# Kernel tuning notes

Hardware: AMD Instinct MI355X
Metric: run time of the kernel (lower is better)

The kernel has to match this reference:

```python
import jax, jax.numpy as jnp
import numpy as np

DIM = 2048
N_HEADS = 32
N_KV_HEADS = 8
HEAD_DIM = DIM // N_HEADS  # 64
N_REP = N_HEADS // N_KV_HEADS  # 4
B, S = 1, 2048


def _rope(t, cos, sin):
    # t: (b, s, h, head_dim); cos/sin: (s, head_dim//2)
    tr = t.reshape(*t.shape[:-1], -1, 2)
    a, b = tr[..., 0], tr[..., 1]
    c = cos[None, :, None, :]
    s_ = sin[None, :, None, :]
    ra = a * c - b * s_
    rb = a * s_ + b * c
    return jnp.stack([ra, rb], axis=-1).reshape(t.shape)


def setup_inputs() -> dict:
    key = jax.random.key(0)
    ks = jax.random.split(key, 6)
    sc = 1.0 / np.sqrt(DIM)
    x = jax.random.normal(ks[0], (B, S, DIM), dtype=jnp.float32)
    wq = jax.random.normal(ks[1], (DIM, N_HEADS * HEAD_DIM), dtype=jnp.float32) * sc
    wk = jax.random.normal(ks[2], (DIM, N_KV_HEADS * HEAD_DIM), dtype=jnp.float32) * sc
    wv = jax.random.normal(ks[3], (DIM, N_KV_HEADS * HEAD_DIM), dtype=jnp.float32) * sc
    wo = jax.random.normal(ks[4], (N_HEADS * HEAD_DIM, DIM), dtype=jnp.float32) * sc
    # rotary frequencies (theta = 500000 as in Llama3)
    inv = 1.0 / (500000.0 ** (np.arange(0, HEAD_DIM, 2, dtype=np.float32) / HEAD_DIM))
    ang = np.arange(S, dtype=np.float32)[:, None] * inv[None, :]
    freqs_cos = jnp.asarray(np.cos(ang), dtype=jnp.float32)
    freqs_sin = jnp.asarray(np.sin(ang), dtype=jnp.float32)
    # causal additive mask
    mask = jnp.triu(jnp.full((S, S), -1e9, dtype=jnp.float32), k=1)
    return {"x": x, "wq": wq, "wk": wk, "wv": wv, "wo": wo,
            "freqs_cos": freqs_cos, "freqs_sin": freqs_sin, "mask": mask,
            "start_pos": 0}


def reference(x, wq, wk, wv, wo, freqs_cos, freqs_sin, mask, start_pos):
    b, s, _ = x.shape
    xq = (x @ wq).reshape(b, s, N_HEADS, HEAD_DIM)
    xk = (x @ wk).reshape(b, s, N_KV_HEADS, HEAD_DIM)
    xv = (x @ wv).reshape(b, s, N_KV_HEADS, HEAD_DIM)
    xq = _rope(xq, freqs_cos, freqs_sin)
    xk = _rope(xk, freqs_cos, freqs_sin)
    # GQA without repeat_interleave: view queries as (b, s, kv, rep, d)
    q = xq.reshape(b, s, N_KV_HEADS, N_REP, HEAD_DIM)
    scale = 1.0 / np.sqrt(HEAD_DIM)
    # scores: (b, kv, rep, q, k)
    scores = jnp.einsum('bqkrd,bskd->bkrqs', q, xk) * scale
    scores = scores + mask[None, None, None, :, :]
    probs = jax.nn.softmax(scores.astype(jnp.float32), axis=-1).astype(x.dtype)
    out = jnp.einsum('bkrqs,bskd->bqkrd', probs, xv)
    out = out.reshape(b, s, N_HEADS * HEAD_DIM)
    return out @ wo
```

## Files before the change

kernel.cpp:

```cpp
#include <hip/hip_runtime.h>
#include <hip/hip_bf16.h>

#define DIM 2048
#define S_LEN 2048
#define N_HEADS 32
#define N_KV_HEADS 8
#define HEAD_DIM 64
#define KV_DIM (N_KV_HEADS * HEAD_DIM)
#define QKV_N (DIM + 2 * KV_DIM)
#define QSCALE 0.18033688011112042f

typedef __attribute__((ext_vector_type(8))) short bf16x8;
typedef __attribute__((ext_vector_type(4))) float f32x4;

__device__ __forceinline__ unsigned short bf16_of(float f) {
    __hip_bfloat16 h = __float2bfloat16(f);
    return *reinterpret_cast<unsigned short*>(&h);
}
__device__ __forceinline__ float f_of_bf16(unsigned short u) {
    unsigned int x = ((unsigned int)u) << 16;
    return __uint_as_float(x);
}
__device__ __forceinline__ void gl_lds16(const void* g, void* l) {
    __builtin_amdgcn_global_load_lds((const __attribute__((address_space(1))) void*)g,
                                     (__attribute__((address_space(3))) void*)l, 16, 0, 0);
}
__device__ __forceinline__ unsigned int pack2tr(float lo, float hi) {
    return __builtin_amdgcn_perm(__float_as_uint(hi), __float_as_uint(lo), 0x07060302u);
}
__device__ __forceinline__ float max3f(float a, float b, float c) {
    float d;
    asm("v_max3_f32 %0, %1, %2, %3" : "=v"(d) : "v"(a), "v"(b), "v"(c));
    return d;
}

__global__ __launch_bounds__(256) void prep(const float* __restrict__ x,
                                            const float* __restrict__ wq,
                                            const float* __restrict__ wk,
                                            const float* __restrict__ wv,
                                            const float* __restrict__ wo,
                                            unsigned short* __restrict__ xbf,
                                            unsigned short* __restrict__ wqkvT,
                                            unsigned short* __restrict__ woT) {
    __shared__ float tile[64][65];
    const int t = threadIdx.x;
    int b = blockIdx.x;
    if (b < 4096) {
        int idx = b * 256 + t;
        float4 f = ((const float4*)x)[idx];
        ushort4 u;
        u.x = bf16_of(f.x); u.y = bf16_of(f.y); u.z = bf16_of(f.z); u.w = bf16_of(f.w);
        ((ushort4*)xbf)[idx] = u;
        return;
    }
    b -= 4096;
    const float* src;
    unsigned short* dst;
    int src_cols, bx, by;
    if (b < 1024)      { src = wq; dst = wqkvT;                                src_cols = DIM;    bx = b & 31;          by = b >> 5; }
    else if (b < 1280) { src = wk; dst = wqkvT + (size_t)DIM * DIM;            src_cols = KV_DIM; bx = (b - 1024) & 7;  by = (b - 1024) >> 3; }
    else if (b < 1536) { src = wv; dst = wqkvT + (size_t)(DIM + KV_DIM) * DIM; src_cols = KV_DIM; bx = (b - 1280) & 7;  by = (b - 1280) >> 3; }
    else               { src = wo; dst = woT;                                  src_cols = DIM;    bx = (b - 1536) & 31; by = (b - 1536) >> 5; }
    const int c0 = bx * 64, r0 = by * 64;
#pragma unroll
    for (int i = 0; i < 4; i++) {
        int idx = t + i * 256;
        int r = idx >> 4, c4 = (idx & 15) * 4;
        float4 f = *(const float4*)&src[(size_t)(r0 + r) * src_cols + c0 + c4];
        tile[r][c4 + 0] = f.x; tile[r][c4 + 1] = f.y;
        tile[r][c4 + 2] = f.z; tile[r][c4 + 3] = f.w;
    }
    __syncthreads();
#pragma unroll
    for (int i = 0; i < 4; i++) {
        int idx = t + i * 256;
        int rr = idx >> 4, cc = (idx & 15) * 4;
        ushort4 u;
        u.x = bf16_of(tile[cc + 0][rr]);
        u.y = bf16_of(tile[cc + 1][rr]);
        u.z = bf16_of(tile[cc + 2][rr]);
        u.w = bf16_of(tile[cc + 3][rr]);
        *(ushort4*)&dst[(size_t)(c0 + rr) * DIM + r0 + cc] = u;
    }
}

__global__ __launch_bounds__(256) void gemm_bt64(const unsigned short* __restrict__ A,
                                                 const unsigned short* __restrict__ Bt,
                                                 void* __restrict__ Cv,
                                                 unsigned short* __restrict__ kbf,
                                                 unsigned short* __restrict__ vbt,
                                                 const float* __restrict__ fcos,
                                                 const float* __restrict__ fsin,
                                                 int M, int N, int K, int mode) {
    __shared__ unsigned short As[2][128 * 64];
    __shared__ unsigned short Bs[2][64 * 64];
    const int tid = threadIdx.x;
    const int wave = tid >> 6, lane = tid & 63;
    const int m16 = lane & 15, quad = lane >> 4;
    const int m0 = blockIdx.y * 128, n0 = blockIdx.x * 64;
    const int wm = (wave >> 1) * 64, wn = (wave & 1) * 32;

    const int lrow = lane >> 3;
    const int gc = (lane & 7) ^ lrow;
    const unsigned short* Ab = A + (size_t)(m0 + wave * 8 + lrow) * K + gc * 8;
    const unsigned short* Bb = Bt + (size_t)(n0 + wave * 8 + lrow) * K + gc * 8;

    f32x4 acc[4][2];
#pragma unroll
    for (int mb = 0; mb < 4; mb++)
#pragma unroll
        for (int nb = 0; nb < 2; nb++) acc[mb][nb] = (f32x4){0.f, 0.f, 0.f, 0.f};

#pragma unroll
    for (int g = 0; g < 4; g++)
        gl_lds16(Ab + (size_t)g * 32 * K, &As[0][(g * 32 + wave * 8) * 64]);
#pragma unroll
    for (int g = 0; g < 2; g++)
        gl_lds16(Bb + (size_t)g * 32 * K, &Bs[0][(g * 32 + wave * 8) * 64]);

    const int nt = K >> 6;
    for (int kt = 0; kt < nt; kt++) {
        __syncthreads();
        if (kt + 1 < nt) {
            const int nb2 = (kt + 1) & 1;
            const int k0 = (kt + 1) << 6;
#pragma unroll
            for (int g = 0; g < 4; g++)
                gl_lds16(Ab + (size_t)g * 32 * K + k0, &As[nb2][(g * 32 + wave * 8) * 64]);
#pragma unroll
            for (int g = 0; g < 2; g++)
                gl_lds16(Bb + (size_t)g * 32 * K + k0, &Bs[nb2][(g * 32 + wave * 8) * 64]);
        }
        const unsigned short* A_ = As[kt & 1];
        const unsigned short* B_ = Bs[kt & 1];
#pragma unroll
        for (int ks = 0; ks < 2; ks++) {
            const int ch = (ks * 4 + quad) ^ (m16 & 7);
            bf16x8 af[4], bfr[2];
#pragma unroll
            for (int mb = 0; mb < 4; mb++)
                af[mb] = *(const bf16x8*)&A_[(wm + mb * 16 + m16) * 64 + ch * 8];
#pragma unroll
            for (int nb = 0; nb < 2; nb++)
                bfr[nb] = *(const bf16x8*)&B_[(wn + nb * 16 + m16) * 64 + ch * 8];
#pragma unroll
            for (int mb = 0; mb < 4; mb++)
#pragma unroll
                for (int nb = 0; nb < 2; nb++)
                    acc[mb][nb] = __builtin_amdgcn_mfma_f32_16x16x32_bf16(af[mb], bfr[nb], acc[mb][nb], 0, 0, 0);
        }
    }

    if (mode == 0) {
        float* C = (float*)Cv;
#pragma unroll
        for (int mb = 0; mb < 4; mb++)
#pragma unroll
            for (int nb = 0; nb < 2; nb++)
#pragma unroll
                for (int r = 0; r < 4; r++)
                    C[(size_t)(m0 + wm + mb * 16 + quad * 4 + r) * N + n0 + wn + nb * 16 + m16] =
                        acc[mb][nb][r];
    } else if (n0 < DIM) {
        unsigned short* C = (unsigned short*)Cv;
#pragma unroll
        for (int mb = 0; mb < 4; mb++)
#pragma unroll
            for (int nb = 0; nb < 2; nb++)
#pragma unroll
                for (int r = 0; r < 4; r++)
                    C[(size_t)(m0 + wm + mb * 16 + quad * 4 + r) * N + n0 + wn + nb * 16 + m16] =
                        bf16_of(acc[mb][nb][r]);
    } else if (n0 < DIM + KV_DIM) {
        const int even = !(m16 & 1);
#pragma unroll
        for (int mb = 0; mb < 4; mb++)
#pragma unroll
            for (int nb = 0; nb < 2; nb++) {
                const int khd  = n0 - DIM + wn + nb * 16 + m16;
                const int pair = ((wn + nb * 16 + m16) & 63) >> 1;
#pragma unroll
                for (int r = 0; r < 4; r++) {
                    const int s = m0 + wm + mb * 16 + quad * 4 + r;
                    float v = acc[mb][nb][r];
                    float p = __shfl_xor(v, 1, 64);
                    float c  = fcos[s * 32 + pair];
                    float sn = fsin[s * 32 + pair];
                    float res = even ? (v * c - p * sn) : (v * c + p * sn);
                    kbf[(size_t)s * KV_DIM + khd] = bf16_of(res);
                }
            }
    } else {
#pragma unroll
        for (int mb = 0; mb < 4; mb++)
#pragma unroll
            for (int nb = 0; nb < 2; nb++) {
                const int d = n0 - DIM - KV_DIM + wn + nb * 16 + m16;
                const int sbase = m0 + wm + mb * 16 + quad * 4;
                const int kl = sbase & 127;
                const int kpb = (kl & 0x60) | ((kl & 0x0C) << 1) | ((kl & 0x10) >> 2);
                ushort4 u;
                u.x = bf16_of(acc[mb][nb][0]);
                u.y = bf16_of(acc[mb][nb][1]);
                u.z = bf16_of(acc[mb][nb][2]);
                u.w = bf16_of(acc[mb][nb][3]);
                *(ushort4*)&vbt[(size_t)d * S_LEN + (sbase & ~127) + kpb] = u;
            }
    }
}

__global__ __launch_bounds__(256) void attn_mfma9(const unsigned short* __restrict__ qkv,
                                                  const unsigned short* __restrict__ kb,
                                                  const unsigned short* __restrict__ vbt,
                                                  const float* __restrict__ fcos,
                                                  const float* __restrict__ fsin,
                                                  unsigned short* __restrict__ out) {
    const int h  = blockIdx.x;
    const int qt = 31 - (int)blockIdx.y;
    const int kh = h >> 2;
    const int tid  = threadIdx.x;
    const int wave = tid >> 6;
    const int lane = tid & 63;
    const int m16  = lane & 15;
    const int quad = lane >> 4;

    __shared__ unsigned short Ks[2][128 * 64];
    __shared__ unsigned short Vt[64 * 128];

    const int lrow8 = lane >> 3;
    const int kc    = (lane & 7) ^ lrow8;
    const int lrow4 = lane >> 4;
    const int vc    = (lane & 15) ^ ((wave * 4 + lrow4) & 7);

    const unsigned short* Kbase = kb + (size_t)kh * 64 + (size_t)(wave * 8 + lrow8) * KV_DIM + kc * 8;
    const unsigned short* Vbase = vbt + (size_t)(kh * 64 + wave * 4 + lrow4) * S_LEN + vc * 8;

    bf16x8 ones;
#pragma unroll
    for (int i = 0; i < 8; i++) ones[i] = (short)0x3F80;

    const int q0 = qt * 64;
    const int n_iter = (qt >> 1) + 1;

    bf16x8 qa[2];
    {
        const int qrow = q0 + wave * 16 + m16;
        const unsigned short* qsrc = qkv + (size_t)qrow * QKV_N + h * 64;
#pragma unroll
        for (int ks = 0; ks < 2; ks++) {
            bf16x8 raw = *(const bf16x8*)&qsrc[ks * 32 + quad * 8];
            float4 c4 = *(const float4*)&fcos[qrow * 32 + ks * 16 + quad * 4];
            float4 s4 = *(const float4*)&fsin[qrow * 32 + ks * 16 + quad * 4];
            float cs[4] = {c4.x, c4.y, c4.z, c4.w};
            float sn[4] = {s4.x, s4.y, s4.z, s4.w};
#pragma unroll
            for (int p = 0; p < 4; p++) {
                float a = f_of_bf16((unsigned short)raw[2 * p]);
                float bb = f_of_bf16((unsigned short)raw[2 * p + 1]);
                qa[ks][2 * p]     = (short)bf16_of((a * cs[p] - bb * sn[p]) * QSCALE);
                qa[ks][2 * p + 1] = (short)bf16_of((a * sn[p] + bb * cs[p]) * QSCALE);
            }
        }
    }

    f32x4 o_acc[4];
#pragma unroll
    for (int nb = 0; nb < 4; nb++) o_acc[nb] = (f32x4){0.f, 0.f, 0.f, 0.f};
    f32x4 l_acc = (f32x4){0.f, 0.f, 0.f, 0.f};
    float m_s = -1e30f;
    const int qrow_lane = q0 + wave * 16 + m16;
    const int orow_base = q0 + wave * 16 + quad * 4;

#pragma unroll
    for (int g = 0; g < 4; g++)
        gl_lds16(Kbase + (size_t)(g * 32) * KV_DIM, &Ks[0][(g * 32 + wave * 8) * 64]);

    for (int kt = 0; kt < n_iter; kt++) {
        asm volatile("s_waitcnt vmcnt(0)" ::: "memory");
        __builtin_amdgcn_s_barrier();
        __builtin_amdgcn_sched_barrier(0);

        const int knext = (kt + 1 < n_iter) ? (kt + 1) : kt;
#pragma unroll
        for (int g = 0; g < 4; g++)
            gl_lds16(Vbase + (size_t)g * 16 * S_LEN + kt * 128,
                     &Vt[(g * 16 + wave * 4) * 128]);
#pragma unroll
        for (int g = 0; g < 4; g++)
            gl_lds16(Kbase + (size_t)(knext * 128 + g * 32) * KV_DIM,
                     &Ks[(kt + 1) & 1][(g * 32 + wave * 8) * 64]);

        const unsigned short* K_ = Ks[kt & 1];

        f32x4 sc[8];
#pragma unroll
        for (int cb = 0; cb < 8; cb++) sc[cb] = (f32x4){0.f, 0.f, 0.f, 0.f};
        __builtin_amdgcn_s_setprio(1);
#pragma unroll
        for (int ks = 0; ks < 2; ks++) {
            const int slot = (ks * 4 + quad) ^ (m16 & 7);
#pragma unroll
            for (int cb = 0; cb < 8; cb++) {
                bf16x8 kf = *(const bf16x8*)&K_[(cb * 16 + m16) * 64 + slot * 8];
                sc[cb] = __builtin_amdgcn_mfma_f32_16x16x32_bf16(kf, qa[ks], sc[cb], 0, 0, 0);
            }
        }
        __builtin_amdgcn_s_setprio(0);

        if (kt == n_iter - 1) {
#pragma unroll
            for (int cb = 0; cb < 8; cb++) {
                int key = kt * 128 + cb * 16 + quad * 4;
#pragma unroll
                for (int r = 0; r < 4; r++)
                    if (key + r > qrow_lane) sc[cb][r] = -1e30f;
            }
        }

        float rmax = fmaxf(sc[0][0], sc[0][1]);
        rmax = max3f(sc[0][2], sc[0][3], rmax);
#pragma unroll
        for (int cb = 1; cb < 8; cb++) {
            rmax = max3f(sc[cb][0], sc[cb][1], rmax);
            rmax = max3f(sc[cb][2], sc[cb][3], rmax);
        }
        rmax = fmaxf(rmax, __shfl_xor(rmax, 16, 64));
        rmax = fmaxf(rmax, __shfl_xor(rmax, 32, 64));

        if (!__all(rmax - m_s <= 8.0f)) {
            float mnew = fmaxf(m_s, rmax);
            float alpha = __builtin_amdgcn_exp2f(m_s - mnew);
            m_s = mnew;
#pragma unroll
            for (int r = 0; r < 4; r++) {
                float a_r = __shfl(alpha, quad * 4 + r, 64);
#pragma unroll
                for (int nb = 0; nb < 4; nb++) o_acc[nb][r] *= a_r;
                l_acc[r] *= a_r;
            }
        }

#pragma unroll
        for (int cb = 0; cb < 8; cb++)
#pragma unroll
            for (int r = 0; r < 4; r++)
                sc[cb][r] = __builtin_amdgcn_exp2f(sc[cb][r] - m_s);

        unsigned int P01[8], P23[8];
#pragma unroll
        for (int cb = 0; cb < 8; cb++) {
            P01[cb] = pack2tr(sc[cb][0], sc[cb][1]);
            P23[cb] = pack2tr(sc[cb][2], sc[cb][3]);
        }

        asm volatile("s_waitcnt vmcnt(4)" ::: "memory");
        __builtin_amdgcn_s_barrier();
        __builtin_amdgcn_sched_barrier(0);

        __builtin_amdgcn_s_setprio(1);
#pragma unroll
        for (int ks = 0; ks < 4; ks++) {
            union { unsigned int u[4]; bf16x8 v; } pa;
            pa.u[0] = P01[2 * ks];     pa.u[1] = P23[2 * ks];
            pa.u[2] = P01[2 * ks + 1]; pa.u[3] = P23[2 * ks + 1];
            const int slot = (ks * 4 + quad) ^ (m16 & 7);
#pragma unroll
            for (int nb = 0; nb < 4; nb++) {
                bf16x8 vf = *(const bf16x8*)&Vt[(nb * 16 + m16) * 128 + slot * 8];
                o_acc[nb] = __builtin_amdgcn_mfma_f32_16x16x32_bf16(pa.v, vf, o_acc[nb], 0, 0, 0);
            }
            l_acc = __builtin_amdgcn_mfma_f32_16x16x32_bf16(pa.v, ones, l_acc, 0, 0, 0);
        }
        __builtin_amdgcn_s_setprio(0);
    }

#pragma unroll
    for (int r = 0; r < 4; r++) {
        float inv_l = 1.f / l_acc[r];
#pragma unroll
        for (int nb = 0; nb < 4; nb++)
            out[(size_t)(orow_base + r) * DIM + h * 64 + nb * 16 + m16] =
                bf16_of(o_acc[nb][r] * inv_l);
    }
}

extern "C" void kernel_launch(void* const* d_in, const int* in_sizes, int n_in,
                              void* d_out, int out_size, void* d_ws, size_t ws_size,
                              hipStream_t stream) {
    const float* x    = (const float*)d_in[0];
    const float* wq   = (const float*)d_in[1];
    const float* wk   = (const float*)d_in[2];
    const float* wv   = (const float*)d_in[3];
    const float* wo   = (const float*)d_in[4];
    const float* fcos = (const float*)d_in[5];
    const float* fsin = (const float*)d_in[6];

    char* ws = (char*)d_ws;
    const size_t MB = 1024 * 1024;
    unsigned short* xbf    = (unsigned short*)(ws);
    unsigned short* wqkvT  = (unsigned short*)(ws + 8 * MB);
    unsigned short* woT    = (unsigned short*)(ws + 20 * MB);
    unsigned short* qkvbf  = (unsigned short*)(ws + 28 * MB);
    unsigned short* vbt    = (unsigned short*)(ws + 40 * MB);
    unsigned short* kbf    = (unsigned short*)(ws + 42 * MB);
    unsigned short* attnbf = (unsigned short*)(ws);

    prep<<<4096 + 2560, 256, 0, stream>>>(x, wq, wk, wv, wo, xbf, wqkvT, woT);

    gemm_bt64<<<dim3(QKV_N / 64, S_LEN / 128), 256, 0, stream>>>(
        xbf, wqkvT, qkvbf, kbf, vbt, fcos, fsin, S_LEN, QKV_N, DIM, 2);

    attn_mfma9<<<dim3(N_HEADS, 32), 256, 0, stream>>>(qkvbf, kbf, vbt, fcos, fsin, attnbf);

    gemm_bt64<<<dim3(DIM / 64, S_LEN / 128), 256, 0, stream>>>(
        attnbf, woT, d_out, nullptr, nullptr, nullptr, nullptr, S_LEN, DIM, DIM, 0);
}
```

Baseline: 213.9 us.

## Load GEMM B fragments directly into registers and hand-schedule A LDS double buffer

In the projection GEMM, the B operand is no longer staged through shared memory. Each wave now loads its B fragments straight from global memory into registers, one tile ahead. The A tile stays double-buffered in LDS, and the k-loop is unrolled by two with explicit vmcnt waits, raw s_barrier and sched_barrier to control overlap. This cuts LDS traffic and footprint, but B rows are read redundantly by waves through the cache with less coalesced 16-byte accesses. The loop also assumes an even tile count.

```diff
diff --git a/kernel.cpp b/kernel.cpp
--- a/kernel.cpp
+++ b/kernel.cpp
@@ -93,7 +93,6 @@
                                                  const float* __restrict__ fsin,
                                                  int M, int N, int K, int mode) {
     __shared__ unsigned short As[2][128 * 64];
-    __shared__ unsigned short Bs[2][64 * 64];
     const int tid = threadIdx.x;
     const int wave = tid >> 6, lane = tid & 63;
     const int m16 = lane & 15, quad = lane >> 4;
@@ -103,7 +102,8 @@
     const int lrow = lane >> 3;
     const int gc = (lane & 7) ^ lrow;
     const unsigned short* Ab = A + (size_t)(m0 + wave * 8 + lrow) * K + gc * 8;
-    const unsigned short* Bb = Bt + (size_t)(n0 + wave * 8 + lrow) * K + gc * 8;
+    const unsigned short* Br0 = Bt + (size_t)(n0 + wn + m16) * K + quad * 8;
+    const unsigned short* Br1 = Bt + (size_t)(n0 + wn + 16 + m16) * K + quad * 8;
 
     f32x4 acc[4][2];
 #pragma unroll
@@ -111,44 +111,55 @@
 #pragma unroll
         for (int nb = 0; nb < 2; nb++) acc[mb][nb] = (f32x4){0.f, 0.f, 0.f, 0.f};
 
-#pragma unroll
-    for (int g = 0; g < 4; g++)
-        gl_lds16(Ab + (size_t)g * 32 * K, &As[0][(g * 32 + wave * 8) * 64]);
-#pragma unroll
-    for (int g = 0; g < 2; g++)
-        gl_lds16(Bb + (size_t)g * 32 * K, &Bs[0][(g * 32 + wave * 8) * 64]);
-
-    const int nt = K >> 6;
-    for (int kt = 0; kt < nt; kt++) {
-        __syncthreads();
-        if (kt + 1 < nt) {
-            const int nb2 = (kt + 1) & 1;
-            const int k0 = (kt + 1) << 6;
-#pragma unroll
-            for (int g = 0; g < 4; g++)
-                gl_lds16(Ab + (size_t)g * 32 * K + k0, &As[nb2][(g * 32 + wave * 8) * 64]);
-#pragma unroll
-            for (int g = 0; g < 2; g++)
-                gl_lds16(Bb + (size_t)g * 32 * K + k0, &Bs[nb2][(g * 32 + wave * 8) * 64]);
-        }
-        const unsigned short* A_ = As[kt & 1];
-        const unsigned short* B_ = Bs[kt & 1];
+    bf16x8 b0[2][2], b1[2][2];
+
+    auto STAGEA = [&](int t, int bufi) {
+        const int k0 = t << 6;
+#pragma unroll
+        for (int g = 0; g < 4; g++)
+            gl_lds16(Ab + (size_t)g * 32 * K + k0, &As[bufi][(g * 32 + wave * 8) * 64]);
+    };
+    auto LOADB = [&](int t, bf16x8 (&bb)[2][2]) {
+        const int k0 = t << 6;
+#pragma unroll
+        for (int ks = 0; ks < 2; ks++) {
+            bb[ks][0] = *(const bf16x8*)&Br0[k0 + ks * 32];
+            bb[ks][1] = *(const bf16x8*)&Br1[k0 + ks * 32];
+        }
+    };
+    auto COMPUTE = [&](const unsigned short* A_, bf16x8 (&bb)[2][2]) {
 #pragma unroll
         for (int ks = 0; ks < 2; ks++) {
             const int ch = (ks * 4 + quad) ^ (m16 & 7);
-            bf16x8 af[4], bfr[2];
+            bf16x8 af[4];
 #pragma unroll
             for (int mb = 0; mb < 4; mb++)
                 af[mb] = *(const bf16x8*)&A_[(wm + mb * 16 + m16) * 64 + ch * 8];
 #pragma unroll
-            for (int nb = 0; nb < 2; nb++)
-                bfr[nb] = *(const bf16x8*)&B_[(wn + nb * 16 + m16) * 64 + ch * 8];
-#pragma unroll
-            for (int mb = 0; mb < 4; mb++)
-#pragma unroll
-                for (int nb = 0; nb < 2; nb++)
-                    acc[mb][nb] = __builtin_amdgcn_mfma_f32_16x16x32_bf16(af[mb], bfr[nb], acc[mb][nb], 0, 0, 0);
-        }
+            for (int mb = 0; mb < 4; mb++) {
+                acc[mb][0] = __builtin_amdgcn_mfma_f32_16x16x32_bf16(af[mb], bb[ks][0], acc[mb][0], 0, 0, 0);
+                acc[mb][1] = __builtin_amdgcn_mfma_f32_16x16x32_bf16(af[mb], bb[ks][1], acc[mb][1], 0, 0, 0);
+            }
+        }
+    };
+
+    STAGEA(0, 0);
+    LOADB(0, b0);
+
+    const int nt = K >> 6;
+    for (int kt = 0; kt < nt; kt += 2) {
+        asm volatile("s_waitcnt vmcnt(4)" ::: "memory");
+        __builtin_amdgcn_s_barrier();
+        __builtin_amdgcn_sched_barrier(0);
+        STAGEA(kt + 1, 1);
+        LOADB(kt + 1, b1);
+        COMPUTE(As[0], b0);
+
+        asm volatile("s_waitcnt vmcnt(4)" ::: "memory");
+        __builtin_amdgcn_s_barrier();
+        __builtin_amdgcn_sched_barrier(0);
+        if (kt + 2 < nt) { STAGEA(kt + 2, 0); LOADB(kt + 2, b0); }
+        COMPUTE(As[1], b1);
     }
 
     if (mode == 0) {
```

Result: slower. 260.1 us (+21.6%).
